# Kernel tuning notes

Measured on AMD Instinct MI355X. Metric: run time of the kernel, lower is better.

Reference implementation:

```python
import jax, jax.numpy as jnp
import numpy as np

B, S, D, H = 2, 2048, 1024, 16
HD = D // H  # 64


def setup_inputs() -> dict:
    key = jax.random.key(0)
    ks = jax.random.split(key, 7)
    s = 1.0 / np.sqrt(HD)
    return {
        "x": jax.random.normal(ks[0], (B, S, D), dtype=jnp.float32),
        "Wq": jax.random.normal(ks[1], (H, HD, HD), dtype=jnp.float32) * s,
        "bq": jax.random.normal(ks[2], (H, HD), dtype=jnp.float32) * 0.01,
        "Wk": jax.random.normal(ks[3], (H, HD, HD), dtype=jnp.float32) * s,
        "bk": jax.random.normal(ks[4], (H, HD), dtype=jnp.float32) * 0.01,
        "Wv": jax.random.normal(ks[5], (H, HD, HD), dtype=jnp.float32) * s,
        "bv": jax.random.normal(ks[6], (H, HD), dtype=jnp.float32) * 0.01,
    }


def reference(x, Wq, bq, Wk, bk, Wv, bv):
    b, s, d = x.shape
    h, hd, _ = Wq.shape
    # Faithful to torch: x.view(B, H, S, hd) is a raw reshape (mixes seq positions
    # across heads), NOT a transpose-based head split.
    xh = x.reshape(b, h, s, hd)
    # torch Linear: y @ W.T + b, with W of shape (out, in)
    q = jnp.einsum('bhse,hde->bhsd', xh, Wq) + bq[None, :, None, :]
    k = jnp.einsum('bhse,hde->bhsd', xh, Wk) + bk[None, :, None, :]
    v = jnp.einsum('bhse,hde->bhsd', xh, Wv) + bv[None, :, None, :]
    scale = 1.0 / jnp.sqrt(jnp.asarray(d / h, dtype=jnp.float32))
    attn = jax.nn.softmax(jnp.einsum('bhqd,bhkd->bhqk', q, k) * scale, axis=-1)
    out = jnp.einsum('bhqk,bhkd->bhqd', attn, v)
    # torch.cat over heads along last dim == transpose then merge
    return out.transpose(0, 2, 1, 3).reshape(b, s, d)
```

## Files before the change

kernel.cpp:

```cpp
#include <hip/hip_runtime.h>
#include <hip/hip_bf16.h>

#define BATCH 2
#define SEQ   2048
#define DMODEL 1024
#define NH    16
#define HD    64
#define QSCALE 0.1803368801111602f

typedef __attribute__((ext_vector_type(8))) short bf16x8;
typedef __attribute__((ext_vector_type(4))) float f32x4;

__device__ __forceinline__ ushort f2bf(float f) {
    union { float f; unsigned u; } v; v.f = f;
    return (ushort)((v.u + 0x8000u) >> 16);
}

__device__ __forceinline__ unsigned pack2bf(float a, float b) {
    union { float f; unsigned u; } x, y; x.f = a; y.f = b;
    return __builtin_amdgcn_perm(y.u + 0x8000u, x.u + 0x8000u, 0x07060302u);
}

__device__ __forceinline__ float exp2r(float x) {
#if __has_builtin(__builtin_amdgcn_exp2f)
    return __builtin_amdgcn_exp2f(x);
#else
    return exp2f(x);
#endif
}

#define MFMA(a, b, c) __builtin_amdgcn_mfma_f32_16x16x32_bf16((a), (b), (c), 0, 0, 0)

__global__ __launch_bounds__(256) void wfmt_kernel(
    const float* __restrict__ Wq, const float* __restrict__ Wk,
    const float* __restrict__ Wv, ushort* __restrict__ Wf)
{
    const int blk = blockIdx.x;
    const int h = blk / 3, m = blk - h * 3;
    const float* W = (m == 0 ? Wq : (m == 1 ? Wk : Wv)) + h * 4096;
    const float s = (m == 0) ? QSCALE : 1.0f;
    for (int i = 0; i < 2; ++i) {
        int idx = threadIdx.x + 256 * i;
        int l = idx & 63, chunk = idx >> 6;
        int qd = l >> 4, l16 = l & 15, nt = chunk >> 1, ks = chunk & 1;
        const float* src = W + (nt * 16 + l16) * 64 + ks * 32 + qd * 8;
        float4 a = *(const float4*)src;
        float4 b = *(const float4*)(src + 4);
        union { bf16x8 v; unsigned u[4]; } t;
        t.u[0] = pack2bf(a.x * s, a.y * s);
        t.u[1] = pack2bf(a.z * s, a.w * s);
        t.u[2] = pack2bf(b.x * s, b.y * s);
        t.u[3] = pack2bf(b.z * s, b.w * s);
        *(bf16x8*)&Wf[((size_t)blk * 512 + idx) * 8] = t.v;
    }
}

__global__ __launch_bounds__(256) void qkv_kernel(
    const float* __restrict__ x, const ushort* __restrict__ Wf,
    const float* __restrict__ bq, const float* __restrict__ bk,
    const float* __restrict__ bv,
    ushort* __restrict__ Qo, ushort* __restrict__ Kf, ushort* __restrict__ Vf)
{
    const int bid = blockIdx.x;
    const int st  = bid & 31;
    const int bh  = bid >> 5;
    const int h   = bh & (NH - 1);

    __shared__ ushort EbQ[64 * 72];
    __shared__ ushort EbK[64 * 72];
    __shared__ ushort EbV[64 * 72];

    const int tid  = threadIdx.x;
    const int wave = tid >> 6, lane = tid & 63;
    const int ln16 = lane & 15, quad = lane >> 4;

    const float* xr = x + (size_t)bh * (SEQ * HD)
                        + ((size_t)st * 64 + wave * 16 + ln16) * HD;
    bf16x8 afr[2];
#pragma unroll
    for (int ks = 0; ks < 2; ++ks) {
        const float4* p = (const float4*)(xr + ks * 32 + quad * 8);
        float4 a = p[0], b = p[1];
        union { bf16x8 v; unsigned u[4]; } t;
        t.u[0] = pack2bf(a.x, a.y);
        t.u[1] = pack2bf(a.z, a.w);
        t.u[2] = pack2bf(b.x, b.y);
        t.u[3] = pack2bf(b.z, b.w);
        afr[ks] = t.v;
    }

    const bf16x8* wf = (const bf16x8*)Wf + (size_t)h * 1536 + lane;

    f32x4 acc[3][4];
#pragma unroll
    for (int m = 0; m < 3; ++m)
#pragma unroll
        for (int nt = 0; nt < 4; ++nt) {
            f32x4 a = {0.f, 0.f, 0.f, 0.f};
            a = MFMA(afr[0], wf[(m * 8 + nt * 2 + 0) * 64], a);
            a = MFMA(afr[1], wf[(m * 8 + nt * 2 + 1) * 64], a);
            acc[m][nt] = a;
        }

#pragma unroll
    for (int nt = 0; nt < 4; ++nt) {
        float bbq = bq[h * 64 + nt * 16 + ln16] * QSCALE;
        float bbk = bk[h * 64 + nt * 16 + ln16];
#pragma unroll
        for (int r = 0; r < 4; ++r) {
            EbQ[(wave * 16 + quad * 4 + r) * 72 + nt * 16 + ln16] = f2bf(acc[0][nt][r] + bbq);
            EbK[(wave * 16 + quad * 4 + r) * 72 + nt * 16 + ln16] = f2bf(acc[1][nt][r] + bbk);
        }
        float bbv = bv[h * 64 + nt * 16 + ln16];
        ushort4 o;
        o.x = f2bf(acc[2][nt][0] + bbv);
        o.y = f2bf(acc[2][nt][1] + bbv);
        o.z = f2bf(acc[2][nt][2] + bbv);
        o.w = f2bf(acc[2][nt][3] + bbv);
        *(ushort4*)&EbV[(nt * 16 + ln16) * 72 + wave * 16 + quad * 4] = o;
    }
    __syncthreads();

    {
        ushort* dst = Qo + (size_t)bh * SEQ * HD + (size_t)st * 64 * HD;
        for (int i = 0; i < 2; ++i) {
            int idx = tid + 256 * i;
            int row = idx >> 3, c8 = (idx & 7) * 8;
            *(bf16x8*)&dst[row * 64 + c8] = *(const bf16x8*)&EbQ[row * 72 + c8];
        }
    }
    {
        ushort* dstK = Kf + ((size_t)bh * 32 + st) * 4096;
        ushort* dstV = Vf + ((size_t)bh * 32 + st) * 4096;
        for (int i = 0; i < 2; ++i) {
            int idx8 = tid + 256 * i;
            int l2 = idx8 & 63, chunk = idx8 >> 6;
            int nt = chunk >> 1, ks = chunk & 1;
            int qd = l2 >> 4, l16 = l2 & 15;
            *(bf16x8*)&dstK[(size_t)idx8 * 8] =
                *(const bf16x8*)&EbK[(nt * 16 + l16) * 72 + ks * 32 + qd * 8];
            *(bf16x8*)&dstV[(size_t)idx8 * 8] =
                *(const bf16x8*)&EbV[(nt * 16 + l16) * 72 + ks * 32 + qd * 8];
        }
    }
}

__global__ __launch_bounds__(512, 2) void attn_kernel(
    const ushort* __restrict__ Q, const ushort* __restrict__ Kf,
    const ushort* __restrict__ Vf, float* __restrict__ out)
{
    const int bid = blockIdx.x;
    const int wid = (bid & 7) * 64 + (bid >> 3);
    const int qt  = wid & 15;
    const int bh  = wid >> 4;
    const int h   = bh & (NH - 1), b = bh >> 4;

    __shared__ ushort Ps[8][2][2048];

    const int tid = threadIdx.x, wave = tid >> 6, lane = tid & 63;
    const int ln16 = lane & 15, quad = lane >> 4;
    const int qw = wave & 3, kh = wave >> 2;
    const unsigned swz = (unsigned)(ln16 & 7) << 4;

    bf16x8 qfr[2][2];
#pragma unroll
    for (int g = 0; g < 2; ++g) {
        const ushort* Qg = Q + ((size_t)bh * SEQ + qt * 128 + qw * 32 + g * 16 + ln16) * HD;
        qfr[g][0] = *(const bf16x8*)&Qg[quad * 8];
        qfr[g][1] = *(const bf16x8*)&Qg[32 + quad * 8];
    }

    const bf16x8* kfp = (const bf16x8*)(Kf + (size_t)bh * 32 * 4096) + kh * 8192 + lane;
    const bf16x8* vfp = (const bf16x8*)(Vf + (size_t)bh * 32 * 4096) + kh * 8192 + lane;

    float lsum[2] = {0.f, 0.f};
    f32x4 accO[2][4];
#pragma unroll
    for (int g = 0; g < 2; ++g)
#pragma unroll
        for (int nt = 0; nt < 4; ++nt) accO[g][nt] = (f32x4){0.f, 0.f, 0.f, 0.f};

    bf16x8 kf[8], vf[8];
#pragma unroll
    for (int c = 0; c < 8; ++c) kf[c] = kfp[c * 64];
    kfp += 512;

    for (int kt = 0; kt < 16; ++kt) {
        const int cur = kt & 1;

        f32x4 sacc[2][4];
#pragma unroll
        for (int nt = 0; nt < 4; ++nt)
#pragma unroll
            for (int g = 0; g < 2; ++g) {
                f32x4 a = {0.f, 0.f, 0.f, 0.f};
                a = MFMA(kf[nt * 2],     qfr[g][0], a);
                a = MFMA(kf[nt * 2 + 1], qfr[g][1], a);
                sacc[g][nt] = a;
            }

        if (kt < 15) {
#pragma unroll
            for (int c = 0; c < 8; ++c) kf[c] = kfp[c * 64];
            kfp += 512;
        }

        if (kt > 0) {
            const char* Pr = (const char*)Ps[wave][1 - cur];
            bf16x8 pf[2][2];
#pragma unroll
            for (int g = 0; g < 2; ++g) {
                const char* Prr = Pr + (g * 16 + ln16) * 128;
                pf[g][0] = *(const bf16x8*)(Prr + (((unsigned)(quad * 16)) ^ swz));
                pf[g][1] = *(const bf16x8*)(Prr + (((unsigned)(64 + quad * 16)) ^ swz));
            }
#pragma unroll
            for (int nt = 0; nt < 4; ++nt)
#pragma unroll
                for (int g = 0; g < 2; ++g) {
                    accO[g][nt] = MFMA(vf[nt * 2],     pf[g][0], accO[g][nt]);
                    accO[g][nt] = MFMA(vf[nt * 2 + 1], pf[g][1], accO[g][nt]);
                }
        }

#pragma unroll
        for (int c = 0; c < 8; ++c) vf[c] = vfp[c * 64];
        vfp += 512;

        char* Pw = (char*)Ps[wave][cur];
#pragma unroll
        for (int g = 0; g < 2; ++g) {
            char* Pwr = Pw + (g * 16 + ln16) * 128;
            float rs = 0.f;
#pragma unroll
            for (int nt = 0; nt < 4; ++nt) {
                float p0 = exp2r(sacc[g][nt][0]);
                float p1 = exp2r(sacc[g][nt][1]);
                float p2 = exp2r(sacc[g][nt][2]);
                float p3 = exp2r(sacc[g][nt][3]);
                rs += (p0 + p1) + (p2 + p3);
                uint2 pk;
                pk.x = pack2bf(p0, p1);
                pk.y = pack2bf(p2, p3);
                *(uint2*)(Pwr + (((unsigned)(nt * 32 + quad * 8)) ^ swz)) = pk;
            }
            lsum[g] += rs;
        }
    }

    {
        const char* Pr = (const char*)Ps[wave][1];
        bf16x8 pf[2][2];
#pragma unroll
        for (int g = 0; g < 2; ++g) {
            const char* Prr = Pr + (g * 16 + ln16) * 128;
            pf[g][0] = *(const bf16x8*)(Prr + (((unsigned)(quad * 16)) ^ swz));
            pf[g][1] = *(const bf16x8*)(Prr + (((unsigned)(64 + quad * 16)) ^ swz));
        }
#pragma unroll
        for (int nt = 0; nt < 4; ++nt)
#pragma unroll
            for (int g = 0; g < 2; ++g) {
                accO[g][nt] = MFMA(vf[nt * 2],     pf[g][0], accO[g][nt]);
                accO[g][nt] = MFMA(vf[nt * 2 + 1], pf[g][1], accO[g][nt]);
            }
    }

    __syncthreads();
    if (kh == 1) {
        float* ex = (float*)&Ps[wave][0][0];
#pragma unroll
        for (int g = 0; g < 2; ++g)
#pragma unroll
            for (int nt = 0; nt < 4; ++nt)
                *(f32x4*)&ex[((g * 4 + nt) * 64 + lane) * 4] = accO[g][nt];
        float* exl = (float*)&Ps[wave - 4][0][0];
        exl[lane * 2 + 0] = lsum[0];
        exl[lane * 2 + 1] = lsum[1];
    }
    __syncthreads();
    if (kh == 0) {
        const float* ex  = (const float*)&Ps[wave + 4][0][0];
        const float* exl = (const float*)&Ps[wave][0][0];
#pragma unroll
        for (int g = 0; g < 2; ++g)
#pragma unroll
            for (int nt = 0; nt < 4; ++nt) {
                f32x4 o = *(const f32x4*)&ex[((g * 4 + nt) * 64 + lane) * 4];
                accO[g][nt][0] += o[0]; accO[g][nt][1] += o[1];
                accO[g][nt][2] += o[2]; accO[g][nt][3] += o[3];
            }
        lsum[0] += exl[lane * 2 + 0];
        lsum[1] += exl[lane * 2 + 1];

#pragma unroll
        for (int g = 0; g < 2; ++g) {
            float l = lsum[g];
            l += __shfl_xor(l, 16, 64);
            l += __shfl_xor(l, 32, 64);
            float rinv = 1.0f / l;
            float* ob = out + ((size_t)b * SEQ + qt * 128 + qw * 32 + g * 16 + ln16) * DMODEL + h * HD;
#pragma unroll
            for (int nt = 0; nt < 4; ++nt) {
                float4 o;
                o.x = accO[g][nt][0] * rinv;
                o.y = accO[g][nt][1] * rinv;
                o.z = accO[g][nt][2] * rinv;
                o.w = accO[g][nt][3] * rinv;
                *(float4*)&ob[nt * 16 + quad * 4] = o;
            }
        }
    }
}

extern "C" void kernel_launch(void* const* d_in, const int* in_sizes, int n_in,
                              void* d_out, int out_size, void* d_ws, size_t ws_size,
                              hipStream_t stream) {
    const float* x  = (const float*)d_in[0];
    const float* Wq = (const float*)d_in[1];
    const float* bq = (const float*)d_in[2];
    const float* Wk = (const float*)d_in[3];
    const float* bk = (const float*)d_in[4];
    const float* Wv = (const float*)d_in[5];
    const float* bv = (const float*)d_in[6];

    const size_t nElem = (size_t)BATCH * NH * SEQ * HD;
    ushort* Qw  = (ushort*)d_ws;
    ushort* Kw  = Qw + nElem;
    ushort* Vw  = Kw + nElem;
    ushort* Wfw = Vw + nElem;

    wfmt_kernel<<<48, 256, 0, stream>>>(Wq, Wk, Wv, Wfw);
    qkv_kernel<<<32 * 32, 256, 0, stream>>>(
        x, Wfw, bq, bk, bv, Qw, Kw, Vw);
    attn_kernel<<<BATCH * NH * (SEQ / 128), 512, 0, stream>>>(
        Qw, Kw, Vw, (float*)d_out);
}
```

Before: 128.4 us.

## Drop split-K waves in attention, use padded P layout and MFMA priority

The attention kernel moves from 8 waves (two halves of the key range, merged through shared memory) to 4 waves that each walk all 32 key tiles. This removes the cross-wave reduction, its two block barriers and the workgroup swizzle. The XOR-swizzled P buffer becomes a row-padded layout (stride 72), and s_setprio is raised around the MFMA blocks. Each block now has half the waves and a serial loop twice as long, which lowers the latency hiding available per CU.

```diff
diff --git a/kernel.cpp b/kernel.cpp
--- a/kernel.cpp
+++ b/kernel.cpp
@@ -145,33 +145,30 @@
     }
 }
 
-__global__ __launch_bounds__(512, 2) void attn_kernel(
+__global__ __launch_bounds__(256, 2) void attn_kernel(
     const ushort* __restrict__ Q, const ushort* __restrict__ Kf,
     const ushort* __restrict__ Vf, float* __restrict__ out)
 {
     const int bid = blockIdx.x;
-    const int wid = (bid & 7) * 64 + (bid >> 3);
-    const int qt  = wid & 15;
-    const int bh  = wid >> 4;
+    const int qt  = bid & 15;
+    const int bh  = bid >> 4;
     const int h   = bh & (NH - 1), b = bh >> 4;
 
-    __shared__ ushort Ps[8][2][2048];
+    __shared__ ushort Ps[4][2][32 * 72];
 
     const int tid = threadIdx.x, wave = tid >> 6, lane = tid & 63;
     const int ln16 = lane & 15, quad = lane >> 4;
-    const int qw = wave & 3, kh = wave >> 2;
-    const unsigned swz = (unsigned)(ln16 & 7) << 4;
 
     bf16x8 qfr[2][2];
 #pragma unroll
     for (int g = 0; g < 2; ++g) {
-        const ushort* Qg = Q + ((size_t)bh * SEQ + qt * 128 + qw * 32 + g * 16 + ln16) * HD;
+        const ushort* Qg = Q + ((size_t)bh * SEQ + qt * 128 + wave * 32 + g * 16 + ln16) * HD;
         qfr[g][0] = *(const bf16x8*)&Qg[quad * 8];
         qfr[g][1] = *(const bf16x8*)&Qg[32 + quad * 8];
     }
 
-    const bf16x8* kfp = (const bf16x8*)(Kf + (size_t)bh * 32 * 4096) + kh * 8192 + lane;
-    const bf16x8* vfp = (const bf16x8*)(Vf + (size_t)bh * 32 * 4096) + kh * 8192 + lane;
+    const bf16x8* kfp = (const bf16x8*)(Kf + (size_t)bh * 32 * 4096) + lane;
+    const bf16x8* vfp = (const bf16x8*)(Vf + (size_t)bh * 32 * 4096) + lane;
 
     float lsum[2] = {0.f, 0.f};
     f32x4 accO[2][4];
@@ -185,10 +182,11 @@
     for (int c = 0; c < 8; ++c) kf[c] = kfp[c * 64];
     kfp += 512;
 
-    for (int kt = 0; kt < 16; ++kt) {
+    for (int kt = 0; kt < 32; ++kt) {
         const int cur = kt & 1;
 
         f32x4 sacc[2][4];
+        __builtin_amdgcn_s_setprio(1);
 #pragma unroll
         for (int nt = 0; nt < 4; ++nt)
 #pragma unroll
@@ -198,22 +196,23 @@
                 a = MFMA(kf[nt * 2 + 1], qfr[g][1], a);
                 sacc[g][nt] = a;
             }
-
-        if (kt < 15) {
+        __builtin_amdgcn_s_setprio(0);
+
+        if (kt < 31) {
 #pragma unroll
             for (int c = 0; c < 8; ++c) kf[c] = kfp[c * 64];
             kfp += 512;
         }
 
         if (kt > 0) {
-            const char* Pr = (const char*)Ps[wave][1 - cur];
+            const ushort* Pr = Ps[wave][1 - cur];
             bf16x8 pf[2][2];
 #pragma unroll
             for (int g = 0; g < 2; ++g) {
-                const char* Prr = Pr + (g * 16 + ln16) * 128;
-                pf[g][0] = *(const bf16x8*)(Prr + (((unsigned)(quad * 16)) ^ swz));
-                pf[g][1] = *(const bf16x8*)(Prr + (((unsigned)(64 + quad * 16)) ^ swz));
+                pf[g][0] = *(const bf16x8*)&Pr[(g * 16 + ln16) * 72 + quad * 8];
+                pf[g][1] = *(const bf16x8*)&Pr[(g * 16 + ln16) * 72 + 32 + quad * 8];
             }
+            __builtin_amdgcn_s_setprio(1);
 #pragma unroll
             for (int nt = 0; nt < 4; ++nt)
 #pragma unroll
@@ -221,16 +220,16 @@
                     accO[g][nt] = MFMA(vf[nt * 2],     pf[g][0], accO[g][nt]);
                     accO[g][nt] = MFMA(vf[nt * 2 + 1], pf[g][1], accO[g][nt]);
                 }
+            __builtin_amdgcn_s_setprio(0);
         }
 
 #pragma unroll
         for (int c = 0; c < 8; ++c) vf[c] = vfp[c * 64];
         vfp += 512;
 
-        char* Pw = (char*)Ps[wave][cur];
+        ushort* Pw = Ps[wave][cur];
 #pragma unroll
         for (int g = 0; g < 2; ++g) {
-            char* Pwr = Pw + (g * 16 + ln16) * 128;
             float rs = 0.f;
 #pragma unroll
             for (int nt = 0; nt < 4; ++nt) {
@@ -242,20 +241,19 @@
                 uint2 pk;
                 pk.x = pack2bf(p0, p1);
                 pk.y = pack2bf(p2, p3);
-                *(uint2*)(Pwr + (((unsigned)(nt * 32 + quad * 8)) ^ swz)) = pk;
+                *(uint2*)&Pw[(g * 16 + ln16) * 72 + nt * 16 + quad * 4] = pk;
             }
             lsum[g] += rs;
         }
     }
 
     {
-        const char* Pr = (const char*)Ps[wave][1];
+        const ushort* Pr = Ps[wave][31 & 1];
         bf16x8 pf[2][2];
 #pragma unroll
         for (int g = 0; g < 2; ++g) {
-            const char* Prr = Pr + (g * 16 + ln16) * 128;
-            pf[g][0] = *(const bf16x8*)(Prr + (((unsigned)(quad * 16)) ^ swz));
-            pf[g][1] = *(const bf16x8*)(Prr + (((unsigned)(64 + quad * 16)) ^ swz));
+            pf[g][0] = *(const bf16x8*)&Pr[(g * 16 + ln16) * 72 + quad * 8];
+            pf[g][1] = *(const bf16x8*)&Pr[(g * 16 + ln16) * 72 + 32 + quad * 8];
         }
 #pragma unroll
         for (int nt = 0; nt < 4; ++nt)
@@ -266,49 +264,21 @@
             }
     }
 
-    __syncthreads();
-    if (kh == 1) {
-        float* ex = (float*)&Ps[wave][0][0];
-#pragma unroll
-        for (int g = 0; g < 2; ++g)
-#pragma unroll
-            for (int nt = 0; nt < 4; ++nt)
-                *(f32x4*)&ex[((g * 4 + nt) * 64 + lane) * 4] = accO[g][nt];
-        float* exl = (float*)&Ps[wave - 4][0][0];
-        exl[lane * 2 + 0] = lsum[0];
-        exl[lane * 2 + 1] = lsum[1];
-    }
-    __syncthreads();
-    if (kh == 0) {
-        const float* ex  = (const float*)&Ps[wave + 4][0][0];
-        const float* exl = (const float*)&Ps[wave][0][0];
-#pragma unroll
-        for (int g = 0; g < 2; ++g)
-#pragma unroll
-            for (int nt = 0; nt < 4; ++nt) {
-                f32x4 o = *(const f32x4*)&ex[((g * 4 + nt) * 64 + lane) * 4];
-                accO[g][nt][0] += o[0]; accO[g][nt][1] += o[1];
-                accO[g][nt][2] += o[2]; accO[g][nt][3] += o[3];
-            }
-        lsum[0] += exl[lane * 2 + 0];
-        lsum[1] += exl[lane * 2 + 1];
-
-#pragma unroll
-        for (int g = 0; g < 2; ++g) {
-            float l = lsum[g];
-            l += __shfl_xor(l, 16, 64);
-            l += __shfl_xor(l, 32, 64);
-            float rinv = 1.0f / l;
-            float* ob = out + ((size_t)b * SEQ + qt * 128 + qw * 32 + g * 16 + ln16) * DMODEL + h * HD;
-#pragma unroll
-            for (int nt = 0; nt < 4; ++nt) {
-                float4 o;
-                o.x = accO[g][nt][0] * rinv;
-                o.y = accO[g][nt][1] * rinv;
-                o.z = accO[g][nt][2] * rinv;
-                o.w = accO[g][nt][3] * rinv;
-                *(float4*)&ob[nt * 16 + quad * 4] = o;
-            }
+#pragma unroll
+    for (int g = 0; g < 2; ++g) {
+        float l = lsum[g];
+        l += __shfl_xor(l, 16, 64);
+        l += __shfl_xor(l, 32, 64);
+        float rinv = 1.0f / l;
+        float* ob = out + ((size_t)b * SEQ + qt * 128 + wave * 32 + g * 16 + ln16) * DMODEL + h * HD;
+#pragma unroll
+        for (int nt = 0; nt < 4; ++nt) {
+            float4 o;
+            o.x = accO[g][nt][0] * rinv;
+            o.y = accO[g][nt][1] * rinv;
+            o.z = accO[g][nt][2] * rinv;
+            o.w = accO[g][nt][3] * rinv;
+            *(float4*)&ob[nt * 16 + quad * 4] = o;
         }
     }
 }
@@ -333,6 +303,6 @@
     wfmt_kernel<<<48, 256, 0, stream>>>(Wq, Wk, Wv, Wfw);
     qkv_kernel<<<32 * 32, 256, 0, stream>>>(
         x, Wfw, bq, bk, bv, Qw, Kw, Vw);
-    attn_kernel<<<BATCH * NH * (SEQ / 128), 512, 0, stream>>>(
+    attn_kernel<<<BATCH * NH * (SEQ / 128), 256, 0, stream>>>(
         Qw, Kw, Vw, (float*)d_out);
 }
```

Result: no change. 130.3 us (+1.5%).
